# Optimization experiments

Measured on AMD Instinct MI355X. Metric: run time of the kernel, lower is better.

The kernel has to match this reference:

```python
import jax, jax.numpy as jnp
import numpy as np

T = 0.07
MOMENTUM = 0.5
B, D = 128, 128
N = 200000
K1 = 2048  # K + 1


def setup_inputs() -> dict:
    key = jax.random.key(0)
    ks = jax.random.split(key, 12)
    stdv = 1.0 / np.sqrt(D / 3.0)
    def bank(k):
        return jax.random.uniform(k, (N, D), dtype=jnp.float32) * (2 * stdv) - stdv
    l = jax.random.normal(ks[0], (B, D), dtype=jnp.float32)
    ab = jax.random.normal(ks[1], (B, D), dtype=jnp.float32)
    ori = jax.random.normal(ks[2], (B, D), dtype=jnp.float32)
    comp = jax.random.normal(ks[3], (B, D), dtype=jnp.float32)
    y = jax.random.randint(ks[4], (B,), 0, N, dtype=jnp.int32)
    idx = jax.random.randint(ks[5], (B, K1), 0, N, dtype=jnp.int32)
    idx = idx.at[:, 0].set(y)  # positive sample in slot 0
    return {
        'l': l, 'ab': ab, 'ori': ori, 'comp': comp, 'y': y, 'idx': idx,
        'memory_l': bank(ks[6]), 'memory_ab': bank(ks[7]),
        'memory_ori': bank(ks[8]), 'memory_comp': bank(ks[9]),
    }


def reference(l, ab, ori, comp, y, idx, memory_l, memory_ab, memory_ori, memory_comp):
    flat = idx.reshape(-1)
    # gather (B*K1, D) rows then fold back to (B, K1, D); weights are detached in torch
    w_l = jax.lax.stop_gradient(memory_l[flat]).reshape(B, K1, D)
    w_ab = jax.lax.stop_gradient(memory_ab[flat]).reshape(B, K1, D)
    w_ori = jax.lax.stop_gradient(memory_ori[flat]).reshape(B, K1, D)
    w_comp = jax.lax.stop_gradient(memory_comp[flat]).reshape(B, K1, D)

    dot = lambda w, v: jnp.einsum('bkd,bd->bk', w, v) / T  # use_softmax path
    out_ab_l = dot(w_l, ab)
    out_l_ori = dot(w_ori, l)
    out_ori_ab = dot(w_ab, ori)
    out_ab_comp = dot(w_comp, ab)
    out_l_comp = dot(w_comp, l)
    out_comp_ori = dot(w_ori, comp)
    outs = jnp.stack([out_l_ori, out_ab_l, out_ori_ab,
                      out_ab_comp, out_l_comp, out_comp_ori])[..., None]  # [6,B,K1,1]

    def ema_update(mem, v):
        pos = mem[y] * MOMENTUM + v * (1.0 - MOMENTUM)
        pos = pos / jnp.sqrt(jnp.sum(pos * pos, axis=1, keepdims=True))
        return mem.at[y].set(pos)

    return (outs,
            ema_update(memory_l, l),
            ema_update(memory_ab, ab),
            ema_update(memory_ori, ori),
            ema_update(memory_comp, comp))
```

## Files before the change

### kernel.cpp

```cpp
#include <hip/hip_runtime.h>

#define BB 128
#define DD 128
#define KK1 2048
#define NROWS 200000

static constexpr float INV_T = 1.0f / 0.07f;
static constexpr float MOM = 0.5f;

typedef float f4 __attribute__((ext_vector_type(4)));

#define COPY_BLOCKS 8192
#define OUTS_BLOCKS 32768
#define TOTAL_BLOCKS (COPY_BLOCKS * 5)

__global__ __launch_bounds__(256) void fused_kernel(
    const float* __restrict__ l, const float* __restrict__ ab,
    const float* __restrict__ ori, const float* __restrict__ comp,
    const int* __restrict__ idx,
    const float* __restrict__ ml, const float* __restrict__ mab,
    const float* __restrict__ mori, const float* __restrict__ mcomp,
    float* __restrict__ outs,
    float* __restrict__ ol, float* __restrict__ oab,
    float* __restrict__ oori, float* __restrict__ ocomp) {
  const int bid = blockIdx.x;
  const int q = bid / 5;
  const int r = bid - q * 5;

  if (r == 2) {
    const int n = NROWS * DD / 4;
    const int stride = COPY_BLOCKS * 256;
    const f4* s0 = (const f4*)ml;
    const f4* s1 = (const f4*)mab;
    const f4* s2 = (const f4*)mori;
    const f4* s3 = (const f4*)mcomp;
    f4* d0 = (f4*)ol;
    f4* d1 = (f4*)oab;
    f4* d2 = (f4*)oori;
    f4* d3 = (f4*)ocomp;
    for (int i = q * 256 + threadIdx.x; i < n; i += stride) {
      f4 a0 = s0[i];
      f4 a1 = s1[i];
      f4 a2 = s2[i];
      f4 a3 = s3[i];
      __builtin_nontemporal_store(a0, d0 + i);
      __builtin_nontemporal_store(a1, d1 + i);
      __builtin_nontemporal_store(a2, d2 + i);
      __builtin_nontemporal_store(a3, d3 + i);
    }
    return;
  }

  const int ob = bid - q - (r > 2 ? 1 : 0);
  const int lane = threadIdx.x & 63;
  const int hl = lane & 31;
  const int w = ob * 8 + ((threadIdx.x >> 6) << 1) + (lane >> 5);
  const int b = w >> 11;

  const int row = idx[w];
  const size_t roff = (size_t)row * DD;

  const f4 wl    = ((const f4*)(ml    + roff))[hl];
  const f4 wab   = ((const f4*)(mab   + roff))[hl];
  const f4 wori  = ((const f4*)(mori  + roff))[hl];
  const f4 wcomp = ((const f4*)(mcomp + roff))[hl];

  const size_t voff = (size_t)b * DD;
  const f4 vl    = ((const f4*)(l    + voff))[hl];
  const f4 vab   = ((const f4*)(ab   + voff))[hl];
  const f4 vori  = ((const f4*)(ori  + voff))[hl];
  const f4 vcomp = ((const f4*)(comp + voff))[hl];

  float d0 = wori[0]*vl[0]    + wori[1]*vl[1]    + wori[2]*vl[2]    + wori[3]*vl[3];
  float d1 = wl[0]*vab[0]     + wl[1]*vab[1]     + wl[2]*vab[2]     + wl[3]*vab[3];
  float d2 = wab[0]*vori[0]   + wab[1]*vori[1]   + wab[2]*vori[2]   + wab[3]*vori[3];
  float d3 = wcomp[0]*vab[0]  + wcomp[1]*vab[1]  + wcomp[2]*vab[2]  + wcomp[3]*vab[3];
  float d4 = wcomp[0]*vl[0]   + wcomp[1]*vl[1]   + wcomp[2]*vl[2]   + wcomp[3]*vl[3];
  float d5 = wori[0]*vcomp[0] + wori[1]*vcomp[1] + wori[2]*vcomp[2] + wori[3]*vcomp[3];

#pragma unroll
  for (int m = 16; m > 0; m >>= 1) {
    d0 += __shfl_xor(d0, m);
    d1 += __shfl_xor(d1, m);
    d2 += __shfl_xor(d2, m);
    d3 += __shfl_xor(d3, m);
    d4 += __shfl_xor(d4, m);
    d5 += __shfl_xor(d5, m);
  }

  if (hl == 0) {
    const int BK = BB * KK1;
    outs[0 * BK + w] = d0 * INV_T;
    outs[1 * BK + w] = d1 * INV_T;
    outs[2 * BK + w] = d2 * INV_T;
    outs[3 * BK + w] = d3 * INV_T;
    outs[4 * BK + w] = d4 * INV_T;
    outs[5 * BK + w] = d5 * INV_T;
  }
}

__global__ __launch_bounds__(64) void ema_kernel(
    const float* __restrict__ l, const float* __restrict__ ab,
    const float* __restrict__ ori, const float* __restrict__ comp,
    const int* __restrict__ y,
    const float* __restrict__ ml, const float* __restrict__ mab,
    const float* __restrict__ mori, const float* __restrict__ mcomp,
    float* __restrict__ ol, float* __restrict__ oab,
    float* __restrict__ oori, float* __restrict__ ocomp) {
  const int b = blockIdx.x;
  const int bank = blockIdx.y;
  const int row = y[b];
  for (int b2 = b + 1; b2 < BB; ++b2)
    if (y[b2] == row) return;

  const float* v;
  const float* mem;
  float* out;
  switch (bank) {
    case 0: v = l;    mem = ml;    out = ol;    break;
    case 1: v = ab;   mem = mab;   out = oab;   break;
    case 2: v = ori;  mem = mori;  out = oori;  break;
    default: v = comp; mem = mcomp; out = ocomp; break;
  }

  const int lane = threadIdx.x;
  const float2 m2 = ((const float2*)(mem + (size_t)row * DD))[lane];
  const float2 v2 = ((const float2*)(v + (size_t)b * DD))[lane];
  float2 p;
  p.x = m2.x * MOM + v2.x * (1.0f - MOM);
  p.y = m2.y * MOM + v2.y * (1.0f - MOM);

  float ss = p.x * p.x + p.y * p.y;
#pragma unroll
  for (int off = 32; off > 0; off >>= 1) ss += __shfl_down(ss, off);
  ss = __shfl(ss, 0);
  const float inv = 1.0f / sqrtf(ss);

  ((float2*)(out + (size_t)row * DD))[lane] = make_float2(p.x * inv, p.y * inv);
}

extern "C" void kernel_launch(void* const* d_in, const int* in_sizes, int n_in,
                              void* d_out, int out_size, void* d_ws, size_t ws_size,
                              hipStream_t stream) {
  const float* l     = (const float*)d_in[0];
  const float* ab    = (const float*)d_in[1];
  const float* ori   = (const float*)d_in[2];
  const float* comp  = (const float*)d_in[3];
  const int*   y     = (const int*)d_in[4];
  const int*   idx   = (const int*)d_in[5];
  const float* ml    = (const float*)d_in[6];
  const float* mab   = (const float*)d_in[7];
  const float* mori  = (const float*)d_in[8];
  const float* mcomp = (const float*)d_in[9];

  float* out = (float*)d_out;
  const size_t OUTS = (size_t)6 * BB * KK1;
  const size_t BANK = (size_t)NROWS * DD;
  float* o_outs  = out;
  float* o_ml    = out + OUTS;
  float* o_mab   = o_ml + BANK;
  float* o_mori  = o_mab + BANK;
  float* o_mcomp = o_mori + BANK;

  fused_kernel<<<TOTAL_BLOCKS, 256, 0, stream>>>(
      l, ab, ori, comp, idx, ml, mab, mori, mcomp,
      o_outs, o_ml, o_mab, o_mori, o_mcomp);

  {
    dim3 grid(BB, 4);
    ema_kernel<<<grid, 64, 0, stream>>>(l, ab, ori, comp, y,
                                        ml, mab, mori, mcomp,
                                        o_ml, o_mab, o_mori, o_mcomp);
  }
}
```

Baseline: 745.7 us.

## Invert idx into per-row buckets so bank copy pass also computes dots

Adds a small pre-pass that zeroes per-row counters and scatters each (b,k) pair index into a fixed-size bucket per memory-bank row using atomics. A new kernel then streams every bank row once, copies it to the output, and computes the six dot products for every pair referencing that row. This removes the separate random gather of about 262K rows from the four banks. In exchange it adds atomic and bucket traffic and workspace use. Any row referenced more than 16 times would silently lose outputs. The old fused path stays as a fallback when the workspace is too small.

```diff
diff --git a/kernel.cpp b/kernel.cpp
--- a/kernel.cpp
+++ b/kernel.cpp
@@ -4,14 +4,93 @@
 #define DD 128
 #define KK1 2048
 #define NROWS 200000
+#define NPAIR (BB * KK1)
+#define SLOTS 16
 
 static constexpr float INV_T = 1.0f / 0.07f;
 static constexpr float MOM = 0.5f;
 
 typedef float f4 __attribute__((ext_vector_type(4)));
 
+__global__ __launch_bounds__(256) void zero_cnt_kernel(int* __restrict__ cnt) {
+  const int i = blockIdx.x * 256 + threadIdx.x;
+  if (i < NROWS) cnt[i] = 0;
+}
+
+__global__ __launch_bounds__(256) void build_kernel(const int* __restrict__ idx,
+                                                    int* __restrict__ cnt,
+                                                    int* __restrict__ bucket) {
+  const int p = blockIdx.x * 256 + threadIdx.x;
+  const int r = idx[p];
+  const int s = atomicAdd(&cnt[r], 1);
+  if (s < SLOTS) bucket[r * SLOTS + s] = p;
+}
+
+__global__ __launch_bounds__(256) void copy_dots_kernel(
+    const float* __restrict__ l, const float* __restrict__ ab,
+    const float* __restrict__ ori, const float* __restrict__ comp,
+    const int* __restrict__ cnt, const int* __restrict__ bucket,
+    const float* __restrict__ ml, const float* __restrict__ mab,
+    const float* __restrict__ mori, const float* __restrict__ mcomp,
+    float* __restrict__ outs,
+    float* __restrict__ ol, float* __restrict__ oab,
+    float* __restrict__ oori, float* __restrict__ ocomp) {
+  const int lane = threadIdx.x & 63;
+  const int hl = lane & 31;
+  const int half = lane >> 5;
+  const int row = blockIdx.x * 8 + ((threadIdx.x >> 6) << 1) + half;
+  const size_t roff = (size_t)row * DD;
+
+  const f4 wl    = __builtin_nontemporal_load((const f4*)(ml    + roff) + hl);
+  const f4 wab   = __builtin_nontemporal_load((const f4*)(mab   + roff) + hl);
+  const f4 wori  = __builtin_nontemporal_load((const f4*)(mori  + roff) + hl);
+  const f4 wcomp = __builtin_nontemporal_load((const f4*)(mcomp + roff) + hl);
+
+  __builtin_nontemporal_store(wl,    (f4*)(ol    + roff) + hl);
+  __builtin_nontemporal_store(wab,   (f4*)(oab   + roff) + hl);
+  __builtin_nontemporal_store(wori,  (f4*)(oori  + roff) + hl);
+  __builtin_nontemporal_store(wcomp, (f4*)(ocomp + roff) + hl);
+
+  int c = cnt[row];
+  if (c > SLOTS) c = SLOTS;
+  for (int s = 0; s < c; ++s) {
+    const int p = bucket[row * SLOTS + s];
+    const int b = p >> 11;
+    const size_t voff = (size_t)b * DD;
+    const f4 vl    = ((const f4*)(l    + voff))[hl];
+    const f4 vab   = ((const f4*)(ab   + voff))[hl];
+    const f4 vori  = ((const f4*)(ori  + voff))[hl];
+    const f4 vcomp = ((const f4*)(comp + voff))[hl];
+
+    float d0 = wori[0]*vl[0]    + wori[1]*vl[1]    + wori[2]*vl[2]    + wori[3]*vl[3];
+    float d1 = wl[0]*vab[0]     + wl[1]*vab[1]     + wl[2]*vab[2]     + wl[3]*vab[3];
+    float d2 = wab[0]*vori[0]   + wab[1]*vori[1]   + wab[2]*vori[2]   + wab[3]*vori[3];
+    float d3 = wcomp[0]*vab[0]  + wcomp[1]*vab[1]  + wcomp[2]*vab[2]  + wcomp[3]*vab[3];
+    float d4 = wcomp[0]*vl[0]   + wcomp[1]*vl[1]   + wcomp[2]*vl[2]   + wcomp[3]*vl[3];
+    float d5 = wori[0]*vcomp[0] + wori[1]*vcomp[1] + wori[2]*vcomp[2] + wori[3]*vcomp[3];
+
+#pragma unroll
+    for (int m = 16; m > 0; m >>= 1) {
+      d0 += __shfl_xor(d0, m);
+      d1 += __shfl_xor(d1, m);
+      d2 += __shfl_xor(d2, m);
+      d3 += __shfl_xor(d3, m);
+      d4 += __shfl_xor(d4, m);
+      d5 += __shfl_xor(d5, m);
+    }
+
+    if (hl == 0) {
+      outs[0 * NPAIR + p] = d0 * INV_T;
+      outs[1 * NPAIR + p] = d1 * INV_T;
+      outs[2 * NPAIR + p] = d2 * INV_T;
+      outs[3 * NPAIR + p] = d3 * INV_T;
+      outs[4 * NPAIR + p] = d4 * INV_T;
+      outs[5 * NPAIR + p] = d5 * INV_T;
+    }
+  }
+}
+
 #define COPY_BLOCKS 8192
-#define OUTS_BLOCKS 32768
 #define TOTAL_BLOCKS (COPY_BLOCKS * 5)
 
 __global__ __launch_bounds__(256) void fused_kernel(
@@ -89,13 +168,12 @@
   }
 
   if (hl == 0) {
-    const int BK = BB * KK1;
-    outs[0 * BK + w] = d0 * INV_T;
-    outs[1 * BK + w] = d1 * INV_T;
-    outs[2 * BK + w] = d2 * INV_T;
-    outs[3 * BK + w] = d3 * INV_T;
-    outs[4 * BK + w] = d4 * INV_T;
-    outs[5 * BK + w] = d5 * INV_T;
+    outs[0 * NPAIR + w] = d0 * INV_T;
+    outs[1 * NPAIR + w] = d1 * INV_T;
+    outs[2 * NPAIR + w] = d2 * INV_T;
+    outs[3 * NPAIR + w] = d3 * INV_T;
+    outs[4 * NPAIR + w] = d4 * INV_T;
+    outs[5 * NPAIR + w] = d5 * INV_T;
   }
 }
 
@@ -154,7 +232,7 @@
   const float* mcomp = (const float*)d_in[9];
 
   float* out = (float*)d_out;
-  const size_t OUTS = (size_t)6 * BB * KK1;
+  const size_t OUTS = (size_t)6 * NPAIR;
   const size_t BANK = (size_t)NROWS * DD;
   float* o_outs  = out;
   float* o_ml    = out + OUTS;
@@ -162,9 +240,22 @@
   float* o_mori  = o_mab + BANK;
   float* o_mcomp = o_mori + BANK;
 
-  fused_kernel<<<TOTAL_BLOCKS, 256, 0, stream>>>(
-      l, ab, ori, comp, idx, ml, mab, mori, mcomp,
-      o_outs, o_ml, o_mab, o_mori, o_mcomp);
+  const size_t WS_NEEDED = (size_t)NROWS * SLOTS * sizeof(int) + (size_t)NROWS * sizeof(int);
+
+  if (ws_size >= WS_NEEDED) {
+    int* bucket = (int*)d_ws;
+    int* cnt    = bucket + (size_t)NROWS * SLOTS;
+
+    zero_cnt_kernel<<<(NROWS + 255) / 256, 256, 0, stream>>>(cnt);
+    build_kernel<<<NPAIR / 256, 256, 0, stream>>>(idx, cnt, bucket);
+    copy_dots_kernel<<<NROWS / 8, 256, 0, stream>>>(
+        l, ab, ori, comp, cnt, bucket, ml, mab, mori, mcomp,
+        o_outs, o_ml, o_mab, o_mori, o_mcomp);
+  } else {
+    fused_kernel<<<TOTAL_BLOCKS, 256, 0, stream>>>(
+        l, ab, ori, comp, idx, ml, mab, mori, mcomp,
+        o_outs, o_ml, o_mab, o_mori, o_mcomp);
+  }
 
   {
     dim3 grid(BB, 4);
```

Measured after the change: 707.1 us. 1.05x faster.
